# Optimization experiments

Measured on AMD Instinct MI355X. Metric: run time of the kernel, lower is better.

## Reference

```python
import jax, jax.numpy as jnp
import numpy as np

B, N, DIM = 8, 1024, 512
HEADS, DIM_HEAD = 8, 64
INNER = HEADS * DIM_HEAD  # 512
SCALE = DIM_HEAD ** -0.5
EPS = 1e-5


def setup_inputs() -> dict:
    key = jax.random.key(0)
    k = jax.random.split(key, 6)
    x = jax.random.normal(k[0], (B, N, DIM), dtype=jnp.float32)
    gamma = jnp.ones((DIM,), dtype=jnp.float32)
    beta = jnp.zeros((DIM,), dtype=jnp.float32)
    # Linear weights stored as (in, out) so y = x @ W (equivalent to torch x @ W.T)
    W_qk = jax.random.normal(k[1], (DIM, 2 * INNER), dtype=jnp.float32) * (DIM ** -0.5)
    W_v = jax.random.normal(k[2], (DIM, INNER), dtype=jnp.float32) * (DIM ** -0.5)
    W_out = jax.random.normal(k[3], (INNER, DIM), dtype=jnp.float32) * (INNER ** -0.5)
    return {"x": x, "gamma": gamma, "beta": beta, "W_qk": W_qk, "W_v": W_v, "W_out": W_out}


def _layernorm(x, gamma, beta):
    mu = jnp.mean(x, axis=-1, keepdims=True)
    var = jnp.mean(jnp.square(x - mu), axis=-1, keepdims=True)
    return (x - mu) * jax.lax.rsqrt(var + EPS) * gamma + beta


def reference(x, gamma, beta, W_qk, W_v, W_out):
    xn = _layernorm(x, gamma, beta)                       # [B,N,D]
    v = xn @ W_v                                          # [B,N,INNER]
    qk = xn @ W_qk                                        # [B,N,2*INNER]
    q, k = jnp.split(qk, 2, axis=-1)
    # b n (h d) -> b h n d
    q = q.reshape(B, N, HEADS, DIM_HEAD).transpose(0, 2, 1, 3)
    k = k.reshape(B, N, HEADS, DIM_HEAD).transpose(0, 2, 1, 3)
    vh = v.reshape(B, N, HEADS, DIM_HEAD).transpose(0, 2, 1, 3)
    dots = jnp.einsum('bhnd,bhmd->bhnm', q, k) * SCALE    # [B,H,N,N]
    attn = jax.nn.softmax(dots, axis=-1)
    out = jnp.einsum('bhnm,bhmd->bhnd', attn, vh)         # [B,H,N,d]
    out = out.transpose(0, 2, 1, 3).reshape(B, N, INNER)  # b h n d -> b n (h d)
    return out @ W_out                                    # [B,N,DIM]
```

## Files before the change

### kernel.cpp

```cpp
#include <hip/hip_runtime.h>

#define TOK 8192
#define DMODEL 512
#define SEQ 1024
#define NH 8
#define DH 64

typedef _Float16 half8 __attribute__((ext_vector_type(8)));
typedef _Float16 half4v __attribute__((ext_vector_type(4)));
typedef float floatx4 __attribute__((ext_vector_type(4)));

__device__ __forceinline__ void gll16(const void* g, void* l) {
  __builtin_amdgcn_global_load_lds(
      (const __attribute__((address_space(1))) void*)g,
      (__attribute__((address_space(3))) void*)l, 16, 0, 0);
}

__global__ __launch_bounds__(256) void prep_kernel(
    const float* __restrict__ x, const float* __restrict__ gamma,
    const float* __restrict__ beta, _Float16* __restrict__ xn,
    const float* __restrict__ Wqk, const float* __restrict__ Wv,
    const float* __restrict__ Wo, _Float16* __restrict__ WqkvT,
    _Float16* __restrict__ WoutT) {
  __shared__ float t[32][33];
  const int bid = blockIdx.x;
  if (bid < 2048) {
    const int row = bid * 4 + (threadIdx.x >> 6);
    const int tt = threadIdx.x & 63;
    const float* xr = x + (size_t)row * DMODEL;
    const float4 a = *(const float4*)(xr + tt * 4);
    const float4 b = *(const float4*)(xr + 256 + tt * 4);
    float s  = a.x + a.y + a.z + a.w + b.x + b.y + b.z + b.w;
    float ss = a.x*a.x + a.y*a.y + a.z*a.z + a.w*a.w
             + b.x*b.x + b.y*b.y + b.z*b.z + b.w*b.w;
    #pragma unroll
    for (int m = 1; m < 64; m <<= 1) {
      s  += __shfl_xor(s, m);
      ss += __shfl_xor(ss, m);
    }
    const float mean = s * (1.0f / DMODEL);
    const float var  = ss * (1.0f / DMODEL) - mean * mean;
    const float inv  = rsqrtf(var + 1e-5f);
    const float4 g0  = *(const float4*)(gamma + tt * 4);
    const float4 g1  = *(const float4*)(gamma + 256 + tt * 4);
    const float4 be0 = *(const float4*)(beta + tt * 4);
    const float4 be1 = *(const float4*)(beta + 256 + tt * 4);
    half4v o0, o1;
    o0[0] = (_Float16)((a.x - mean) * inv * g0.x + be0.x);
    o0[1] = (_Float16)((a.y - mean) * inv * g0.y + be0.y);
    o0[2] = (_Float16)((a.z - mean) * inv * g0.z + be0.z);
    o0[3] = (_Float16)((a.w - mean) * inv * g0.w + be0.w);
    o1[0] = (_Float16)((b.x - mean) * inv * g1.x + be1.x);
    o1[1] = (_Float16)((b.y - mean) * inv * g1.y + be1.y);
    o1[2] = (_Float16)((b.z - mean) * inv * g1.z + be1.z);
    o1[3] = (_Float16)((b.w - mean) * inv * g1.w + be1.w);
    _Float16* outr = xn + (size_t)row * DMODEL;
    *(half4v*)(outr + tt * 4) = o0;
    *(half4v*)(outr + 256 + tt * 4) = o1;
  } else {
    const int r = bid - 2048;
    const int z = r >> 9;
    const int rem = r & 511;
    const float* W;
    _Float16* dst;
    int N, rowoff;
    if (z == 0)      { W = Wqk; dst = WqkvT; N = 1024; rowoff = 0; }
    else if (z == 1) { W = Wv;  dst = WqkvT; N = 512;  rowoff = 1024; }
    else             { W = Wo;  dst = WoutT; N = 512;  rowoff = 0; }
    const int n0 = (rem & 31) * 32;
    if (n0 >= N) return;
    const int k0 = (rem >> 5) * 32;
    const int tx = threadIdx.x & 31, ty = threadIdx.x >> 5;
    #pragma unroll
    for (int j = 0; j < 4; ++j)
      t[ty + j * 8][tx] = W[(size_t)(k0 + ty + j * 8) * N + n0 + tx];
    __syncthreads();
    #pragma unroll
    for (int j = 0; j < 4; ++j)
      dst[(size_t)(rowoff + n0 + ty + j * 8) * 512 + k0 + tx] =
          (_Float16)t[tx][ty + j * 8];
  }
}

template <int MODE>
__global__ __launch_bounds__(256) void hgemm_kernel(
    const _Float16* __restrict__ A, const _Float16* __restrict__ Bt,
    void* __restrict__ Cout, void* __restrict__ Cout2, int M, int N, int K) {
  __shared__ char smem[49152];
  const int tid = threadIdx.x;
  const int bm = blockIdx.x, bn = blockIdx.y;
  const int wv = tid >> 6, lane = tid & 63;
  const int l15 = lane & 15, g = lane >> 4;
  const int wr = wv >> 1, wc = wv & 1;
  const int rswz = ((l15 >> 1) & 3) << 4;
  const _Float16* Ab = A + (size_t)(bm * 128) * K;
  const _Float16* Bb = Bt + (size_t)(bn * 128) * K;
  const int lrow = lane >> 2;
  const int lchk = (lane & 3) * 16;
  const int ssw = lchk ^ (((lrow >> 1) & 3) << 4);

  #define HG_STAGE(buf, kt)                                                   \
    _Pragma("unroll")                                                         \
    for (int i = 0; i < 2; ++i) {                                             \
      const int rbase = wv * 16 + i * 64;                                     \
      gll16((const char*)(Ab + (size_t)(rbase + lrow) * K + (kt)) + ssw,      \
            smem + (buf) * 16384 + rbase * 64);                               \
      gll16((const char*)(Bb + (size_t)(rbase + lrow) * K + (kt)) + ssw,      \
            smem + (buf) * 16384 + 8192 + rbase * 64);                        \
    }

  floatx4 acc[4][4] = {};
  HG_STAGE(0, 0);
  HG_STAGE(1, 32);
  int cur = 0;
  const int nit = K >> 5;
  for (int it = 0; it < nit; ++it) {
    if (it < nit - 2) asm volatile("s_waitcnt vmcnt(4)" ::: "memory");
    else              asm volatile("s_waitcnt vmcnt(0)" ::: "memory");
    __builtin_amdgcn_s_barrier();
    asm volatile("" ::: "memory");
    const int nxt = cur + 2 >= 3 ? cur - 1 : cur + 2;
    if (it + 2 < nit) { HG_STAGE(nxt, (it + 2) * 32); }
    const char* sb = smem + cur * 16384;
    half8 af[4], bf[4];
    #pragma unroll
    for (int mt = 0; mt < 4; ++mt)
      af[mt] = *(const half8*)(sb + (wr * 64 + mt * 16 + l15) * 64 +
                               (g * 16 ^ rswz));
    #pragma unroll
    for (int nt = 0; nt < 4; ++nt)
      bf[nt] = *(const half8*)(sb + 8192 + (wc * 64 + nt * 16 + l15) * 64 +
                               (g * 16 ^ rswz));
    __builtin_amdgcn_s_setprio(1);
    #pragma unroll
    for (int mt = 0; mt < 4; ++mt)
      #pragma unroll
      for (int nt = 0; nt < 4; ++nt)
        acc[mt][nt] = __builtin_amdgcn_mfma_f32_16x16x32_f16(
            af[mt], bf[nt], acc[mt][nt], 0, 0, 0);
    __builtin_amdgcn_s_setprio(0);
    cur = cur + 1 >= 3 ? 0 : cur + 1;
  }
  #undef HG_STAGE
  const int m0 = bm * 128 + wr * 64;
  const int n0 = bn * 128 + wc * 64;
  if constexpr (MODE == 0) {
    float* C = (float*)Cout;
    #pragma unroll
    for (int mt = 0; mt < 4; ++mt)
      #pragma unroll
      for (int nt = 0; nt < 4; ++nt) {
        const int n = n0 + nt * 16 + l15;
        #pragma unroll
        for (int r = 0; r < 4; ++r)
          C[(size_t)(m0 + mt * 16 + 4 * g + r) * 512 + n] = acc[mt][nt][r];
      }
  } else {
    _Float16* Q = (_Float16*)Cout;
    _Float16* V = (_Float16*)Cout2;
    #pragma unroll
    for (int mt = 0; mt < 4; ++mt) {
      const int mrow = m0 + mt * 16 + 4 * g;
      const int b = mrow >> 10, tok = mrow & 1023;
      #pragma unroll
      for (int nt = 0; nt < 4; ++nt) {
        const int n = n0 + nt * 16 + l15;
        if (n < 1024) {
          #pragma unroll
          for (int r = 0; r < 4; ++r)
            Q[(size_t)(mrow + r) * 1024 + n] = (_Float16)acc[mt][nt][r];
        } else {
          const int cv = n - 1024;
          half4v hv;
          #pragma unroll
          for (int r = 0; r < 4; ++r) hv[r] = (_Float16)acc[mt][nt][r];
          *(half4v*)(V + ((size_t)((b * 8 + (cv >> 6)) * 64 + (cv & 63)) << 10) + tok) = hv;
        }
      }
    }
  }
}

#define QSC 0.18033688f
#define MOFF 5.7707801f

__global__ __launch_bounds__(512) void flash16_kernel(
    const _Float16* __restrict__ qkh, const _Float16* __restrict__ vt,
    _Float16* __restrict__ ao) {
  __shared__ char smem[65536];
  const int bh = blockIdx.x;
  const int qt = blockIdx.y;
  const int b = bh >> 3, h = bh & 7;
  const int tid = threadIdx.x;
  const int wv = tid >> 6, lane = tid & 63;
  const int l15 = lane & 15, g = lane >> 4;
  const int swz = (l15 & 7) << 4;
  const int qrow0 = b * SEQ + qt * 128;

  half8 qf[2];
  {
    const _Float16* qp = qkh + (size_t)(qrow0 + wv * 16 + l15) * 1024 + h * DH;
    qf[0] = *(const half8*)(qp + g * 8);
    qf[1] = *(const half8*)(qp + g * 8 + 32);
    qf[0] *= (_Float16)QSC;
    qf[1] *= (_Float16)QSC;
  }

  float lsum = 0.f;
  floatx4 oacc[4] = {};

  const int lrow = lane >> 3;
  const int lchk = (lane & 7) * 16;
  const int ssw = lchk ^ (lrow << 4);
  const _Float16* kbase = qkh + 512 + h * DH;
  const _Float16* vbase = vt + (size_t)bh * 64 * 1024;
  char* pb = smem + 49152 + wv * 2048 + l15 * 128;

  #define FL_STAGE(buf, kt)                                                   \
    {                                                                         \
      const int krow = b * SEQ + (kt) * 64 + wv * 8 + lrow;                   \
      gll16((const char*)(kbase + (size_t)krow * 1024) + ssw,                 \
            smem + (buf) * 16384 + wv * 1024);                                \
      gll16((const char*)(vbase + (size_t)(wv * 8 + lrow) * 1024 +            \
                          (kt) * 64) + ssw,                                   \
            smem + (buf) * 16384 + 8192 + wv * 1024);                         \
    }

  FL_STAGE(0, 0);
  FL_STAGE(1, 1);
  int cur = 0;
  for (int kt = 0; kt < 16; ++kt) {
    if (kt < 15) asm volatile("s_waitcnt vmcnt(2)" ::: "memory");
    else         asm volatile("s_waitcnt vmcnt(0)" ::: "memory");
    __builtin_amdgcn_s_barrier();
    asm volatile("" ::: "memory");
    const int nxt = cur + 2 >= 3 ? cur - 1 : cur + 2;
    if (kt + 2 < 16) FL_STAGE(nxt, kt + 2);
    const char* sb = smem + cur * 16384;

    floatx4 sacc[4] = {};
    __builtin_amdgcn_s_setprio(1);
    #pragma unroll
    for (int kk = 0; kk < 2; ++kk) {
      #pragma unroll
      for (int mt = 0; mt < 4; ++mt) {
        half8 af = *(const half8*)(sb + (16 * mt + l15) * 128 +
                                   ((g * 16 + kk * 64) ^ swz));
        sacc[mt] = __builtin_amdgcn_mfma_f32_16x16x32_f16(af, qf[kk], sacc[mt], 0, 0, 0);
      }
    }
    __builtin_amdgcn_s_setprio(0);

    float rs = 0.f;
    #pragma unroll
    for (int mt = 0; mt < 4; ++mt) {
      float p0 = exp2f(sacc[mt][0] - MOFF);
      float p1 = exp2f(sacc[mt][1] - MOFF);
      float p2 = exp2f(sacc[mt][2] - MOFF);
      float p3 = exp2f(sacc[mt][3] - MOFF);
      rs += (p0 + p1) + (p2 + p3);
      half4v pv;
      pv[0] = (_Float16)p0; pv[1] = (_Float16)p1;
      pv[2] = (_Float16)p2; pv[3] = (_Float16)p3;
      *(half4v*)(pb + ((32 * mt + 8 * g) ^ swz)) = pv;
    }
    rs += __shfl_xor(rs, 16);
    rs += __shfl_xor(rs, 32);
    lsum += rs;

    __builtin_amdgcn_s_setprio(1);
    #pragma unroll
    for (int kk = 0; kk < 2; ++kk) {
      half8 pf = *(const half8*)(pb + ((g * 16 + kk * 64) ^ swz));
      #pragma unroll
      for (int mt = 0; mt < 4; ++mt) {
        half8 vf = *(const half8*)(sb + 8192 + (16 * mt + l15) * 128 +
                                   ((g * 16 + kk * 64) ^ swz));
        oacc[mt] = __builtin_amdgcn_mfma_f32_16x16x32_f16(vf, pf, oacc[mt], 0, 0, 0);
      }
    }
    __builtin_amdgcn_s_setprio(0);
    cur = cur + 1 >= 3 ? 0 : cur + 1;
  }
  #undef FL_STAGE

  const float inv = 1.0f / lsum;
  _Float16* op = ao + (size_t)(qrow0 + wv * 16 + l15) * 512 + h * DH;
  #pragma unroll
  for (int mt = 0; mt < 4; ++mt) {
    half4v hv;
    hv[0] = (_Float16)(oacc[mt][0] * inv);
    hv[1] = (_Float16)(oacc[mt][1] * inv);
    hv[2] = (_Float16)(oacc[mt][2] * inv);
    hv[3] = (_Float16)(oacc[mt][3] * inv);
    *(half4v*)(op + 16 * mt + 4 * g) = hv;
  }
}

extern "C" void kernel_launch(void* const* d_in, const int* in_sizes, int n_in,
                              void* d_out, int out_size, void* d_ws, size_t ws_size,
                              hipStream_t stream) {
  const float* x     = (const float*)d_in[0];
  const float* gamma = (const float*)d_in[1];
  const float* beta  = (const float*)d_in[2];
  const float* W_qk  = (const float*)d_in[3];
  const float* W_v   = (const float*)d_in[4];
  const float* W_out = (const float*)d_in[5];
  float* out = (float*)d_out;
  char* ws = (char*)d_ws;

  const size_t MB = 1024 * 1024;
  _Float16* xn16  = (_Float16*)ws;
  _Float16* qkh   = (_Float16*)(ws + 8 * MB);
  _Float16* vt    = (_Float16*)(ws + 24 * MB);
  _Float16* ao16  = (_Float16*)(ws + 32 * MB);
  _Float16* WqkvT = (_Float16*)(ws + 40 * MB);
  _Float16* WoutT = (_Float16*)(ws + 42 * MB);

  prep_kernel<<<3584, 256, 0, stream>>>(x, gamma, beta, xn16,
                                        W_qk, W_v, W_out, WqkvT, WoutT);
  hgemm_kernel<3><<<dim3(64, 12), 256, 0, stream>>>(
      xn16, WqkvT, qkh, vt, TOK, 1536, 512);
  flash16_kernel<<<dim3(64, 8), 512, 0, stream>>>(qkh, vt, ao16);
  hgemm_kernel<0><<<dim3(64, 4), 256, 0, stream>>>(
      ao16, WoutT, out, nullptr, TOK, 512, 512);
}
```

Before: 74.45 us.

## Enlarge QKV GEMM tile to 256x128 and split GEMM into specialized kernels

The QKV projection GEMM now uses 256x128 block tiles (8x4 MFMA tiles per wave, 72KB LDS triple-buffered), halving the grid along M to raise operand reuse per LDS load. The output GEMM becomes a separate non-templated kernel with constant K. Separately, the flash kernel's row-sum accumulation is split into four independent partial sums to shorten the dependency chain. The larger tile uses more registers and LDS, which lowers occupancy, and the grid drops to 384 blocks, which may underfill the CUs.

```diff
diff --git a/kernel.cpp b/kernel.cpp
--- a/kernel.cpp
+++ b/kernel.cpp
@@ -82,55 +82,143 @@
   }
 }
 
-template <int MODE>
-__global__ __launch_bounds__(256) void hgemm_kernel(
+__global__ __launch_bounds__(256) void hgemm_qkv(
     const _Float16* __restrict__ A, const _Float16* __restrict__ Bt,
-    void* __restrict__ Cout, void* __restrict__ Cout2, int M, int N, int K) {
+    _Float16* __restrict__ Q, _Float16* __restrict__ V) {
+  __shared__ char smem[73728];
+  const int tid = threadIdx.x;
+  const int bm = blockIdx.x, bn = blockIdx.y;
+  const int wv = tid >> 6, lane = tid & 63;
+  const int l15 = lane & 15, g = lane >> 4;
+  const int wr = wv >> 1, wc = wv & 1;
+  const _Float16* Ab = A + (size_t)(bm * 256) * 512;
+  const _Float16* Bb = Bt + (size_t)(bn * 128) * 512;
+  const int lrow = lane >> 2;
+  const int lchk = (lane & 3) * 16;
+  const int ssw = lchk ^ (((lrow >> 1) & 3) << 4);
+
+  #define QKV_STAGE(buf, kt)                                                  \
+    _Pragma("unroll")                                                         \
+    for (int i = 0; i < 4; ++i)                                               \
+      gll16((const char*)(Ab + (size_t)(wv * 64 + i * 16 + lrow) * 512 +      \
+                          (kt)) + ssw,                                        \
+            smem + (buf) * 24576 + (wv * 64 + i * 16) * 64);                  \
+    _Pragma("unroll")                                                         \
+    for (int i = 0; i < 2; ++i)                                               \
+      gll16((const char*)(Bb + (size_t)(wv * 32 + i * 16 + lrow) * 512 +      \
+                          (kt)) + ssw,                                        \
+            smem + (buf) * 24576 + 16384 + (wv * 32 + i * 16) * 64);
+
+  floatx4 acc[8][4] = {};
+  QKV_STAGE(0, 0);
+  QKV_STAGE(1, 32);
+  int cur = 0;
+  for (int it = 0; it < 16; ++it) {
+    if (it < 14) asm volatile("s_waitcnt vmcnt(6)" ::: "memory");
+    else         asm volatile("s_waitcnt vmcnt(0)" ::: "memory");
+    __builtin_amdgcn_s_barrier();
+    asm volatile("" ::: "memory");
+    const int nxt = cur + 2 >= 3 ? cur - 1 : cur + 2;
+    if (it + 2 < 16) { QKV_STAGE(nxt, (it + 2) * 32); }
+    const char* sb = smem + cur * 24576;
+    half8 af[8], bf[4];
+    #pragma unroll
+    for (int mt = 0; mt < 8; ++mt) {
+      const int row = wr * 128 + mt * 16 + l15;
+      af[mt] = *(const half8*)(sb + row * 64 +
+                               ((g * 16) ^ (((row >> 1) & 3) << 4)));
+    }
+    #pragma unroll
+    for (int nt = 0; nt < 4; ++nt) {
+      const int row = wc * 64 + nt * 16 + l15;
+      bf[nt] = *(const half8*)(sb + 16384 + row * 64 +
+                               ((g * 16) ^ (((row >> 1) & 3) << 4)));
+    }
+    __builtin_amdgcn_s_setprio(1);
+    #pragma unroll
+    for (int mt = 0; mt < 8; ++mt)
+      #pragma unroll
+      for (int nt = 0; nt < 4; ++nt)
+        acc[mt][nt] = __builtin_amdgcn_mfma_f32_16x16x32_f16(
+            af[mt], bf[nt], acc[mt][nt], 0, 0, 0);
+    __builtin_amdgcn_s_setprio(0);
+    cur = cur + 1 >= 3 ? 0 : cur + 1;
+  }
+  #undef QKV_STAGE
+  const int m0 = bm * 256 + wr * 128;
+  const int n0 = bn * 128 + wc * 64;
+  #pragma unroll
+  for (int mt = 0; mt < 8; ++mt) {
+    const int mrow = m0 + mt * 16 + 4 * g;
+    const int b = mrow >> 10, tok = mrow & 1023;
+    #pragma unroll
+    for (int nt = 0; nt < 4; ++nt) {
+      const int n = n0 + nt * 16 + l15;
+      if (n < 1024) {
+        #pragma unroll
+        for (int r = 0; r < 4; ++r)
+          Q[(size_t)(mrow + r) * 1024 + n] = (_Float16)acc[mt][nt][r];
+      } else {
+        const int cv = n - 1024;
+        half4v hv;
+        #pragma unroll
+        for (int r = 0; r < 4; ++r) hv[r] = (_Float16)acc[mt][nt][r];
+        *(half4v*)(V + ((size_t)((b * 8 + (cv >> 6)) * 64 + (cv & 63)) << 10) + tok) = hv;
+      }
+    }
+  }
+}
+
+__global__ __launch_bounds__(256) void hgemm_out(
+    const _Float16* __restrict__ A, const _Float16* __restrict__ Bt,
+    float* __restrict__ C) {
   __shared__ char smem[49152];
   const int tid = threadIdx.x;
   const int bm = blockIdx.x, bn = blockIdx.y;
   const int wv = tid >> 6, lane = tid & 63;
   const int l15 = lane & 15, g = lane >> 4;
   const int wr = wv >> 1, wc = wv & 1;
-  const int rswz = ((l15 >> 1) & 3) << 4;
-  const _Float16* Ab = A + (size_t)(bm * 128) * K;
-  const _Float16* Bb = Bt + (size_t)(bn * 128) * K;
+  const _Float16* Ab = A + (size_t)(bm * 128) * 512;
+  const _Float16* Bb = Bt + (size_t)(bn * 128) * 512;
   const int lrow = lane >> 2;
   const int lchk = (lane & 3) * 16;
   const int ssw = lchk ^ (((lrow >> 1) & 3) << 4);
 
-  #define HG_STAGE(buf, kt)                                                   \
+  #define OUT_STAGE(buf, kt)                                                  \
     _Pragma("unroll")                                                         \
     for (int i = 0; i < 2; ++i) {                                             \
       const int rbase = wv * 16 + i * 64;                                     \
-      gll16((const char*)(Ab + (size_t)(rbase + lrow) * K + (kt)) + ssw,      \
+      gll16((const char*)(Ab + (size_t)(rbase + lrow) * 512 + (kt)) + ssw,    \
             smem + (buf) * 16384 + rbase * 64);                               \
-      gll16((const char*)(Bb + (size_t)(rbase + lrow) * K + (kt)) + ssw,      \
+      gll16((const char*)(Bb + (size_t)(rbase + lrow) * 512 + (kt)) + ssw,    \
             smem + (buf) * 16384 + 8192 + rbase * 64);                        \
     }
 
   floatx4 acc[4][4] = {};
-  HG_STAGE(0, 0);
-  HG_STAGE(1, 32);
+  OUT_STAGE(0, 0);
+  OUT_STAGE(1, 32);
   int cur = 0;
-  const int nit = K >> 5;
-  for (int it = 0; it < nit; ++it) {
-    if (it < nit - 2) asm volatile("s_waitcnt vmcnt(4)" ::: "memory");
-    else              asm volatile("s_waitcnt vmcnt(0)" ::: "memory");
+  for (int it = 0; it < 16; ++it) {
+    if (it < 14) asm volatile("s_waitcnt vmcnt(4)" ::: "memory");
+    else         asm volatile("s_waitcnt vmcnt(0)" ::: "memory");
     __builtin_amdgcn_s_barrier();
     asm volatile("" ::: "memory");
     const int nxt = cur + 2 >= 3 ? cur - 1 : cur + 2;
-    if (it + 2 < nit) { HG_STAGE(nxt, (it + 2) * 32); }
+    if (it + 2 < 16) { OUT_STAGE(nxt, (it + 2) * 32); }
     const char* sb = smem + cur * 16384;
     half8 af[4], bf[4];
     #pragma unroll
-    for (int mt = 0; mt < 4; ++mt)
-      af[mt] = *(const half8*)(sb + (wr * 64 + mt * 16 + l15) * 64 +
-                               (g * 16 ^ rswz));
-    #pragma unroll
-    for (int nt = 0; nt < 4; ++nt)
-      bf[nt] = *(const half8*)(sb + 8192 + (wc * 64 + nt * 16 + l15) * 64 +
-                               (g * 16 ^ rswz));
+    for (int mt = 0; mt < 4; ++mt) {
+      const int row = wr * 64 + mt * 16 + l15;
+      af[mt] = *(const half8*)(sb + row * 64 +
+                               ((g * 16) ^ (((row >> 1) & 3) << 4)));
+    }
+    #pragma unroll
+    for (int nt = 0; nt < 4; ++nt) {
+      const int row = wc * 64 + nt * 16 + l15;
+      bf[nt] = *(const half8*)(sb + 8192 + row * 64 +
+                               ((g * 16) ^ (((row >> 1) & 3) << 4)));
+    }
     __builtin_amdgcn_s_setprio(1);
     #pragma unroll
     for (int mt = 0; mt < 4; ++mt)
@@ -141,44 +229,18 @@
     __builtin_amdgcn_s_setprio(0);
     cur = cur + 1 >= 3 ? 0 : cur + 1;
   }
-  #undef HG_STAGE
+  #undef OUT_STAGE
   const int m0 = bm * 128 + wr * 64;
   const int n0 = bn * 128 + wc * 64;
-  if constexpr (MODE == 0) {
-    float* C = (float*)Cout;
-    #pragma unroll
-    for (int mt = 0; mt < 4; ++mt)
-      #pragma unroll
-      for (int nt = 0; nt < 4; ++nt) {
-        const int n = n0 + nt * 16 + l15;
-        #pragma unroll
-        for (int r = 0; r < 4; ++r)
-          C[(size_t)(m0 + mt * 16 + 4 * g + r) * 512 + n] = acc[mt][nt][r];
-      }
-  } else {
-    _Float16* Q = (_Float16*)Cout;
-    _Float16* V = (_Float16*)Cout2;
-    #pragma unroll
-    for (int mt = 0; mt < 4; ++mt) {
-      const int mrow = m0 + mt * 16 + 4 * g;
-      const int b = mrow >> 10, tok = mrow & 1023;
-      #pragma unroll
-      for (int nt = 0; nt < 4; ++nt) {
-        const int n = n0 + nt * 16 + l15;
-        if (n < 1024) {
-          #pragma unroll
-          for (int r = 0; r < 4; ++r)
-            Q[(size_t)(mrow + r) * 1024 + n] = (_Float16)acc[mt][nt][r];
-        } else {
-          const int cv = n - 1024;
-          half4v hv;
-          #pragma unroll
-          for (int r = 0; r < 4; ++r) hv[r] = (_Float16)acc[mt][nt][r];
-          *(half4v*)(V + ((size_t)((b * 8 + (cv >> 6)) * 64 + (cv & 63)) << 10) + tok) = hv;
-        }
-      }
-    }
-  }
+  #pragma unroll
+  for (int mt = 0; mt < 4; ++mt)
+    #pragma unroll
+    for (int nt = 0; nt < 4; ++nt) {
+      const int n = n0 + nt * 16 + l15;
+      #pragma unroll
+      for (int r = 0; r < 4; ++r)
+        C[(size_t)(m0 + mt * 16 + 4 * g + r) * 512 + n] = acc[mt][nt][r];
+    }
 }
 
 #define QSC 0.18033688f
@@ -251,19 +313,20 @@
     }
     __builtin_amdgcn_s_setprio(0);
 
-    float rs = 0.f;
+    float rsp[4];
     #pragma unroll
     for (int mt = 0; mt < 4; ++mt) {
       float p0 = exp2f(sacc[mt][0] - MOFF);
       float p1 = exp2f(sacc[mt][1] - MOFF);
       float p2 = exp2f(sacc[mt][2] - MOFF);
       float p3 = exp2f(sacc[mt][3] - MOFF);
-      rs += (p0 + p1) + (p2 + p3);
+      rsp[mt] = (p0 + p1) + (p2 + p3);
       half4v pv;
       pv[0] = (_Float16)p0; pv[1] = (_Float16)p1;
       pv[2] = (_Float16)p2; pv[3] = (_Float16)p3;
       *(half4v*)(pb + ((32 * mt + 8 * g) ^ swz)) = pv;
     }
+    float rs = (rsp[0] + rsp[1]) + (rsp[2] + rsp[3]);
     rs += __shfl_xor(rs, 16);
     rs += __shfl_xor(rs, 32);
     lsum += rs;
@@ -319,9 +382,7 @@
 
   prep_kernel<<<3584, 256, 0, stream>>>(x, gamma, beta, xn16,
                                         W_qk, W_v, W_out, WqkvT, WoutT);
-  hgemm_kernel<3><<<dim3(64, 12), 256, 0, stream>>>(
-      xn16, WqkvT, qkh, vt, TOK, 1536, 512);
+  hgemm_qkv<<<dim3(32, 12), 256, 0, stream>>>(xn16, WqkvT, qkh, vt);
   flash16_kernel<<<dim3(64, 8), 512, 0, stream>>>(qkh, vt, ao16);
-  hgemm_kernel<0><<<dim3(64, 4), 256, 0, stream>>>(
-      ao16, WoutT, out, nullptr, TOK, 512, 512);
-}
+  hgemm_out<<<dim3(64, 4), 256, 0, stream>>>(ao16, WoutT, out);
+}
```

Measured after the change: 80.58 us. 8.2% more time.
